# Performance work log

Measured on AMD Instinct MI355X. Metric: run time of the kernel, lower is better.

Reference implementation:

```python
import jax, jax.numpy as jnp
import numpy as np

NUM_HEADS = 16
HEAD_DIM = 128
NUM_KV_HEADS = 8
NUM_KV_GROUPS = 2
HIDDEN = 2048
SCALE = 0.5  # hardcoded in the original SDPA call


def _fixed_sincos_pos(E, H):
    # matches ReusedProjReconstructor._fixed_sincos_pos (H even here)
    half = H // 2
    freq = jnp.exp(-jnp.log(jnp.float32(10000.0)) * jnp.arange(half, dtype=jnp.float32) / half)
    pos = jnp.arange(E, dtype=jnp.float32)[:, None]
    ang = pos * freq[None, :]
    return jnp.concatenate([jnp.sin(ang), jnp.cos(ang)], axis=1)  # [E, H]


def setup_inputs() -> dict:
    key = jax.random.key(0)
    ks = jax.random.split(key, 8)
    B, M, H = 4, 2048, HIDDEN
    kv_dim = NUM_KV_HEADS * HEAD_DIM
    s = 0.02
    return {
        "mem_act": jax.random.normal(ks[0], (B, M, H), jnp.float32),
        "Wq": jax.random.normal(ks[1], (H, H), jnp.float32) * s,
        "bq": jax.random.normal(ks[2], (H,), jnp.float32) * s,
        "Wk": jax.random.normal(ks[3], (kv_dim, H), jnp.float32) * s,
        "bk": jax.random.normal(ks[4], (kv_dim,), jnp.float32) * s,
        "Wv": jax.random.normal(ks[5], (kv_dim, H), jnp.float32) * s,
        "bv": jax.random.normal(ks[6], (kv_dim,), jnp.float32) * s,
        "Wo": jax.random.normal(ks[7], (H, H), jnp.float32) * s,
        "E": 2048,
    }


def reference(mem_act, Wq, bq, Wk, bk, Wv, bv, Wo, E):
    B, M, H = mem_act.shape
    # positional query hidden, shared across batch (q_ln is Identity)
    q_hidden = _fixed_sincos_pos(E, H).astype(mem_act.dtype)  # [E, H]
    q = (q_hidden @ Wq.T + bq).reshape(E, NUM_HEADS, HEAD_DIM)          # [E, nh, hd]
    k = (mem_act @ Wk.T + bk).reshape(B, M, NUM_KV_HEADS, HEAD_DIM)     # [B, M, nkv, hd]
    v = (mem_act @ Wv.T + bv).reshape(B, M, NUM_KV_HEADS, HEAD_DIM)
    # GQA: repeat kv heads (repeat_interleave over head dim)
    k = jnp.repeat(k, NUM_KV_GROUPS, axis=2)  # [B, M, nh, hd]
    v = jnp.repeat(v, NUM_KV_GROUPS, axis=2)
    # non-causal SDPA with scale=0.5, query broadcast over batch
    scores = jnp.einsum("ehd,bmhd->bhem", q, k) * SCALE  # [B, nh, E, M]
    attn = jax.nn.softmax(scores, axis=-1)
    out = jnp.einsum("bhem,bmhd->behd", attn, v).reshape(B, E, H)
    pred = out @ Wo.T  # o_proj (no bias, Qwen2 style)
    return pred
```

## Files before the change

kernel.cpp:

```cpp
#include <hip/hip_runtime.h>
#include <hip/hip_bf16.h>

typedef __attribute__((ext_vector_type(8))) short short8;
typedef __attribute__((ext_vector_type(4))) float f32x4;
typedef __attribute__((ext_vector_type(16))) float f32x16;
typedef unsigned short ushort_t;

__device__ __forceinline__ unsigned short f2bf(float x) {
    unsigned int u = __builtin_bit_cast(unsigned int, x);
    unsigned int r = (u + 0x7fffu + ((u >> 16) & 1u)) >> 16;
    return (unsigned short)r;
}

__device__ __forceinline__ void gload_lds16(const ushort_t* g, ushort_t* l) {
    __builtin_amdgcn_global_load_lds(
        (const __attribute__((address_space(1))) void*)g,
        (__attribute__((address_space(3))) void*)l, 16, 0, 0);
}

#define MFMA16(A, B, C) __builtin_amdgcn_mfma_f32_16x16x32_bf16((A), (B), (C), 0, 0, 0)
#define MFMA32(A, B, C) __builtin_amdgcn_mfma_f32_32x32x16_bf16((A), (B), (C), 0, 0, 0)

__global__ __launch_bounds__(256) void prep_all(const float* __restrict__ im,
                                                const float* __restrict__ iq,
                                                const float* __restrict__ ik,
                                                const float* __restrict__ iv,
                                                const float* __restrict__ io,
                                                ushort_t* __restrict__ om,
                                                ushort_t* __restrict__ oq,
                                                ushort_t* __restrict__ ok,
                                                ushort_t* __restrict__ ov,
                                                ushort_t* __restrict__ oo,
                                                ushort_t* __restrict__ qh) {
    const int bid = blockIdx.x;
    if (bid < 14336) {
        long i = ((long)bid * 256 + threadIdx.x) << 3;
        const float* s;
        ushort_t* d;
        if (i < 16777216)      { s = im + i;              d = om + i; }
        else if (i < 20971520) { s = iq + (i - 16777216); d = oq + (i - 16777216); }
        else if (i < 23068672) { s = ik + (i - 20971520); d = ok + (i - 20971520); }
        else if (i < 25165824) { s = iv + (i - 23068672); d = ov + (i - 23068672); }
        else                   { s = io + (i - 25165824); d = oo + (i - 25165824); }
        const float4* p = (const float4*)s;
        float4 a = p[0], b = p[1];
        short8 o;
        o[0] = (short)f2bf(a.x); o[1] = (short)f2bf(a.y);
        o[2] = (short)f2bf(a.z); o[3] = (short)f2bf(a.w);
        o[4] = (short)f2bf(b.x); o[5] = (short)f2bf(b.y);
        o[6] = (short)f2bf(b.z); o[7] = (short)f2bf(b.w);
        *(short8*)d = o;
    } else {
        int idx = (bid - 14336) * 256 + threadIdx.x;
        int e = idx >> 10, i = idx & 1023;
        float freq = __expf(-9.2103403719761836f * (float)i * (1.0f / 1024.0f));
        float ang = (float)e * freq;
        qh[(size_t)e * 2048 + i]        = f2bf(sinf(ang));
        qh[(size_t)e * 2048 + 1024 + i] = f2bf(cosf(ang));
    }
}

__global__ __launch_bounds__(256) void gemm_q(const ushort_t* __restrict__ A,
                                              const ushort_t* __restrict__ Bw,
                                              const float* __restrict__ bias,
                                              ushort_t* __restrict__ Cout,
                                              int M, int N, int K) {
    __shared__ ushort_t As[128 * 32];
    __shared__ ushort_t Bs[128 * 32];
    const int tid = threadIdx.x;
    const int lane = tid & 63;
    const int wid = tid >> 6;
    const int g = lane >> 4;
    const int r = lane & 15;
    const int wr = wid >> 1, wc = wid & 1;
    const int nbn = N >> 7;
    const int bm = blockIdx.x / nbn, bn = blockIdx.x % nbn;
    const int row0 = bm << 7, col0 = bn << 7;

    f32x4 acc[4][4];
#pragma unroll
    for (int i = 0; i < 4; ++i)
#pragma unroll
        for (int j = 0; j < 4; ++j) acc[i][j] = (f32x4){0.f, 0.f, 0.f, 0.f};

    const int f0 = tid * 8;
    const int r0_ = f0 >> 5, c0_ = f0 & 31;
    const int f1 = (256 + tid) * 8;
    const int r1_ = f1 >> 5, c1_ = f1 & 31;

    for (int k0 = 0; k0 < K; k0 += 32) {
        __syncthreads();
        gload_lds16(A  + (size_t)(row0 + r0_) * K + k0 + c0_, As + f0);
        gload_lds16(A  + (size_t)(row0 + r1_) * K + k0 + c1_, As + f1);
        gload_lds16(Bw + (size_t)(col0 + r0_) * K + k0 + c0_, Bs + f0);
        gload_lds16(Bw + (size_t)(col0 + r1_) * K + k0 + c1_, Bs + f1);
        __syncthreads();
        short8 af[4], bfr[4];
#pragma unroll
        for (int i = 0; i < 4; ++i) {
            af[i]  = *(const short8*)(As + (wr * 64 + i * 16 + r) * 32 + g * 8);
            bfr[i] = *(const short8*)(Bs + (wc * 64 + i * 16 + r) * 32 + g * 8);
        }
#pragma unroll
        for (int i = 0; i < 4; ++i)
#pragma unroll
            for (int j = 0; j < 4; ++j) acc[i][j] = MFMA16(af[i], bfr[j], acc[i][j]);
    }

#pragma unroll
    for (int j = 0; j < 4; ++j) {
        const int col = col0 + wc * 64 + j * 16 + r;
        const float bv = bias[col];
#pragma unroll
        for (int i = 0; i < 4; ++i) {
            const int rowb = row0 + wr * 64 + i * 16 + g * 4;
#pragma unroll
            for (int t = 0; t < 4; ++t) {
                float v = (acc[i][j][t] + bv) * 0.5f;
                Cout[(size_t)(rowb + t) * N + col] = f2bf(v);
            }
        }
    }
}

template <int EPI>
__global__ __launch_bounds__(512, 1) void gemm256(const ushort_t* __restrict__ A,
                                                  const ushort_t* __restrict__ Bw,
                                                  const float* __restrict__ b0,
                                                  const float* __restrict__ b1,
                                                  void* __restrict__ C0,
                                                  void* __restrict__ C1,
                                                  int M, int N, int K) {
    __shared__ ushort_t As[4][256 * 32];
    __shared__ ushort_t Bs[4][256 * 32];
    const int tid = threadIdx.x, lane = tid & 63;
    const int wid = tid >> 6;
    const int q5 = lane & 31, hi = lane >> 5;
    const int wm = wid >> 2, wn = wid & 3;
    const int nbn = N >> 8;
    const int nwg = gridDim.x;
    const int swz = (blockIdx.x & 7) * (nwg >> 3) + (blockIdx.x >> 3);
    const int bm = swz / nbn, bn = swz % nbn;
    const int row0 = bm << 8, col0 = bn << 8;
    const int NT = K >> 5;

    f32x16 acc[4][2];
#pragma unroll
    for (int mi = 0; mi < 4; ++mi)
#pragma unroll
        for (int nj = 0; nj < 2; ++nj)
#pragma unroll
            for (int rr = 0; rr < 16; ++rr) acc[mi][nj][rr] = 0.f;

    auto STAGE_HALF = [&](int buf, int kt, int i) {
        const int k0 = kt << 5;
        const int fb = (i * 512 + tid) << 4;
        const int rp = fb >> 7;
        const int bo = ((fb >> 4) & 7) ^ (rp & 7);
        const int row = rp * 2 + (bo >> 2);
        const int kc = (bo & 3) << 3;
        gload_lds16(A  + (size_t)(row0 + row) * K + k0 + kc, &As[buf][0] + (fb >> 1));
        gload_lds16(Bw + (size_t)(col0 + row) * K + k0 + kc, &Bs[buf][0] + (fb >> 1));
    };

    STAGE_HALF(0, 0, 0); STAGE_HALF(0, 0, 1);
    STAGE_HALF(1, 1, 0); STAGE_HALF(1, 1, 1);
    STAGE_HALF(2, 2, 0); STAGE_HALF(2, 2, 1);
    asm volatile("s_waitcnt vmcnt(8)" ::: "memory");
    __builtin_amdgcn_sched_barrier(0);
    __builtin_amdgcn_s_barrier();
    __builtin_amdgcn_sched_barrier(0);

    for (int t = 0; t < NT; ++t) {
        const int buf = t & 3;
        const char* Ab = (const char*)&As[buf][0];
        const char* Bb = (const char*)&Bs[buf][0];
#pragma unroll
        for (int ph = 0; ph < 2; ++ph) {
            short8 af[4], bfr[2];
#pragma unroll
            for (int nj = 0; nj < 2; ++nj) {
                const int col = wn * 64 + nj * 32 + q5;
                const int rp = col >> 1;
                const int blk = (((col & 1) << 2) + ph * 2 + hi) ^ (rp & 7);
                bfr[nj] = *(const short8*)(Bb + rp * 128 + blk * 16);
            }
#pragma unroll
            for (int mi = 0; mi < 4; ++mi) {
                const int row = wm * 128 + mi * 32 + q5;
                const int rp = row >> 1;
                const int blk = (((row & 1) << 2) + ph * 2 + hi) ^ (rp & 7);
                af[mi] = *(const short8*)(Ab + rp * 128 + blk * 16);
            }
            if (t + 3 < NT) STAGE_HALF((t + 3) & 3, t + 3, ph);
            __builtin_amdgcn_s_setprio(1);
#pragma unroll
            for (int mi = 0; mi < 4; ++mi)
#pragma unroll
                for (int nj = 0; nj < 2; ++nj)
                    acc[mi][nj] = MFMA32(af[mi], bfr[nj], acc[mi][nj]);
            __builtin_amdgcn_s_setprio(0);
        }

        if (t + 3 < NT) {
            asm volatile("s_waitcnt vmcnt(8)" ::: "memory");
        } else if (t + 2 < NT) {
            asm volatile("s_waitcnt vmcnt(4)" ::: "memory");
        } else if (t + 1 < NT) {
            asm volatile("s_waitcnt vmcnt(0)" ::: "memory");
        }
        if (t + 1 < NT) {
            __builtin_amdgcn_sched_barrier(0);
            __builtin_amdgcn_s_barrier();
            __builtin_amdgcn_sched_barrier(0);
        }
    }

#pragma unroll
    for (int mi = 0; mi < 4; ++mi)
#pragma unroll
        for (int nj = 0; nj < 2; ++nj) {
            const int col = col0 + wn * 64 + nj * 32 + q5;
            if (EPI == 2) {
                float* outp = (float*)C0;
#pragma unroll
                for (int rr = 0; rr < 16; ++rr) {
                    const int row = row0 + wm * 128 + mi * 32 + (rr & 3) + 8 * (rr >> 2) + 4 * hi;
                    outp[(size_t)row * N + col] = acc[mi][nj][rr];
                }
            } else {
                if (col < 1024) {
                    const float bv = b0[col];
                    ushort_t* Kp = (ushort_t*)C0;
#pragma unroll
                    for (int rr = 0; rr < 16; ++rr) {
                        const int row = row0 + wm * 128 + mi * 32 + (rr & 3) + 8 * (rr >> 2) + 4 * hi;
                        Kp[(size_t)row * 1024 + col] = f2bf(acc[mi][nj][rr] + bv);
                    }
                } else {
                    const int vcol = col - 1024;
                    const float bv = b1[vcol];
                    ushort_t* Vt = (ushort_t*)C1;
#pragma unroll
                    for (int G = 0; G < 4; ++G) {
                        const int m0 = row0 + wm * 128 + mi * 32 + G * 8 + 4 * hi;
                        const int bb = m0 >> 11;
                        const int mm = m0 & 2047;
                        const size_t vtrow = (size_t)(bb * 8 + (vcol >> 7)) * 128 + (vcol & 127);
                        unsigned int p0 = (unsigned int)f2bf(acc[mi][nj][G * 4 + 0] + bv)
                                        | ((unsigned int)f2bf(acc[mi][nj][G * 4 + 1] + bv) << 16);
                        unsigned int p1 = (unsigned int)f2bf(acc[mi][nj][G * 4 + 2] + bv)
                                        | ((unsigned int)f2bf(acc[mi][nj][G * 4 + 3] + bv) << 16);
                        uint2 pk; pk.x = p0; pk.y = p1;
                        *(uint2*)(Vt + vtrow * 2048 + mm) = pk;
                    }
                }
            }
        }
}

__global__ __launch_bounds__(512, 2) void attn_kernel(const ushort_t* __restrict__ Q,
                                                      const ushort_t* __restrict__ Kg,
                                                      const ushort_t* __restrict__ Vt,
                                                      ushort_t* __restrict__ O) {
    __shared__ ushort_t Ks[2][64 * 128];
    __shared__ ushort_t Vts[2][128 * 64];

    const int tid = threadIdx.x, lane = tid & 63, wid = tid >> 6;
    const int q5 = lane & 31;
    const int hi = lane >> 5;
    const int wq = wid & 3;
    const int wg = (blockIdx.x & 7) * 64 + (blockIdx.x >> 3);
    const int bkvh = wg >> 4;
    const int etile = wg & 15;
    const int b = bkvh >> 3, kvh = bkvh & 7;
    const int h = kvh * 2 + (wid >> 2);
    const int e0 = etile * 128;
    const int qrow = e0 + wq * 32 + q5;

    short8 Qf[8];
    {
        const ushort_t* qp = Q + (size_t)qrow * 2048 + h * 128 + hi * 8;
#pragma unroll
        for (int c = 0; c < 8; ++c) Qf[c] = *(const short8*)(qp + c * 16);
    }

    unsigned aK[2][8];
#pragma unroll
    for (int h2 = 0; h2 < 2; ++h2) {
        const int key = h2 * 32 + q5;
#pragma unroll
        for (int c = 0; c < 8; ++c)
            aK[h2][c] = key * 256 + (((c * 2 + hi) ^ (key & 7)) << 4);
    }
    unsigned aV[4];
#pragma unroll
    for (int c16 = 0; c16 < 4; ++c16)
        aV[c16] = q5 * 128 + (((c16 * 2 + hi) ^ (q5 & 7)) << 4);

    float lrow = 0.f;
    f32x16 oacc[4];
#pragma unroll
    for (int d0 = 0; d0 < 4; ++d0)
#pragma unroll
        for (int r = 0; r < 16; ++r) oacc[d0][r] = 0.f;

    f32x16 Z16;
#pragma unroll
    for (int r = 0; r < 16; ++r) Z16[r] = 0.f;

    const ushort_t* Kbase  = Kg + (size_t)b * 2048 * 1024 + kvh * 128;
    const ushort_t* Vtbase = Vt + (size_t)bkvh * 128 * 2048;

    auto STAGE = [&](int buf, int kv0) {
#pragma unroll
        for (int i = 0; i < 2; ++i) {
            const int fb = (i * 8 + wid) * 1024 + lane * 16;
            const int key = fb >> 8;
            const int blk = (fb >> 4) & 15;
            gload_lds16(Kbase + (size_t)(kv0 + key) * 1024 + ((blk ^ (key & 7)) << 3),
                        &Ks[buf][0] + (fb >> 1));
            const int d = fb >> 7;
            const int kb = (fb >> 4) & 7;
            gload_lds16(Vtbase + (size_t)d * 2048 + kv0 + ((kb ^ (d & 7)) << 3),
                        &Vts[buf][0] + (fb >> 1));
        }
    };

    auto TILE = [&](int bo) {
        f32x16 sS[2];
        __builtin_amdgcn_s_setprio(1);
#pragma unroll
        for (int c = 0; c < 8; ++c) {
            short8 ka0 = *(const short8*)((const char*)Ks + bo + aK[0][c]);
            short8 ka1 = *(const short8*)((const char*)Ks + bo + aK[1][c]);
            sS[0] = MFMA32(ka0, Qf[c], (c == 0) ? Z16 : sS[0]);
            sS[1] = MFMA32(ka1, Qf[c], (c == 0) ? Z16 : sS[1]);
        }
        __builtin_amdgcn_s_setprio(0);

#pragma unroll
        for (int h2 = 0; h2 < 2; ++h2)
#pragma unroll
            for (int r = 0; r < 16; ++r) sS[h2][r] = __expf(sS[h2][r]);

        float ts[16];
#pragma unroll
        for (int i = 0; i < 8; ++i) ts[i] = sS[0][2 * i] + sS[0][2 * i + 1];
#pragma unroll
        for (int i = 0; i < 8; ++i) ts[8 + i] = sS[1][2 * i] + sS[1][2 * i + 1];
#pragma unroll
        for (int s = 8; s > 0; s >>= 1)
#pragma unroll
            for (int i = 0; i < s; ++i) ts[i] += ts[i + s];
        lrow += ts[0] + __shfl_xor(ts[0], 32);

        unsigned int W[2][4][2];
#pragma unroll
        for (int h2 = 0; h2 < 2; ++h2)
#pragma unroll
            for (int q4 = 0; q4 < 4; ++q4)
#pragma unroll
                for (int p = 0; p < 2; ++p) {
                    unsigned int w;
                    asm("v_cvt_pk_bf16_f32 %0, %1, %2"
                        : "=v"(w)
                        : "v"(sS[h2][q4 * 4 + 2 * p]), "v"(sS[h2][q4 * 4 + 2 * p + 1]));
                    W[h2][q4][p] = w;
                }

#pragma unroll
        for (int c16 = 0; c16 < 4; ++c16) {
            const int h2 = c16 >> 1;
            const int q4a = (c16 & 1) * 2, q4b = q4a + 1;
            auto r0 = __builtin_amdgcn_permlane32_swap(W[h2][q4a][0], W[h2][q4b][0], false, false);
            auto r1 = __builtin_amdgcn_permlane32_swap(W[h2][q4a][1], W[h2][q4b][1], false, false);
            union { unsigned int w[4]; short8 v; } pa;
            pa.w[0] = r0[0];
            pa.w[1] = r1[0];
            pa.w[2] = r0[1];
            pa.w[3] = r1[1];
            __builtin_amdgcn_s_setprio(1);
#pragma unroll
            for (int d0 = 0; d0 < 4; ++d0) {
                short8 vb = *(const short8*)((const char*)Vts + bo + aV[c16] + d0 * 4096);
                oacc[d0] = MFMA32(pa.v, vb, oacc[d0]);
            }
            __builtin_amdgcn_s_setprio(0);
        }
    };

    STAGE(0, 0);
    __syncthreads();

#pragma unroll 1
    for (int tt = 0; tt < 16; ++tt) {
        STAGE(1, (2 * tt + 1) * 64);
        TILE(0);
        __syncthreads();
        if (tt < 15) STAGE(0, (2 * tt + 2) * 64);
        TILE(16384);
        __syncthreads();
    }

#pragma unroll
    for (int reg = 0; reg < 16; ++reg) {
        const int qr = (reg & 3) + 8 * (reg >> 2) + 4 * hi;
        const float lr = __shfl(lrow, qr);
        const float inv = 1.0f / lr;
        const int e = e0 + wq * 32 + qr;
        ushort_t* op = O + ((size_t)b * 2048 + e) * 2048 + h * 128 + q5;
#pragma unroll
        for (int d0 = 0; d0 < 4; ++d0)
            op[d0 * 32] = f2bf(oacc[d0][reg] * inv);
    }
}

extern "C" void kernel_launch(void* const* d_in, const int* in_sizes, int n_in,
                              void* d_out, int out_size, void* d_ws, size_t ws_size,
                              hipStream_t stream) {
    const float* mem_act = (const float*)d_in[0];
    const float* Wq = (const float*)d_in[1];
    const float* bq = (const float*)d_in[2];
    const float* Wk = (const float*)d_in[3];
    const float* bk = (const float*)d_in[4];
    const float* Wv = (const float*)d_in[5];
    const float* bv = (const float*)d_in[6];
    const float* Wo = (const float*)d_in[7];
    float* out = (float*)d_out;

    char* w = (char*)d_ws;
    ushort_t* memb = (ushort_t*)w; w += (size_t)16777216 * 2;
    ushort_t* wqb  = (ushort_t*)w; w += (size_t)4194304 * 2;
    ushort_t* wkvb = (ushort_t*)w; w += (size_t)4194304 * 2;
    ushort_t* wob  = (ushort_t*)w; w += (size_t)4194304 * 2;
    ushort_t* qh   = (ushort_t*)w; w += (size_t)4194304 * 2;
    ushort_t* Qp   = (ushort_t*)w; w += (size_t)4194304 * 2;
    ushort_t* Kp   = (ushort_t*)w; w += (size_t)8388608 * 2;
    ushort_t* Vtp  = (ushort_t*)w; w += (size_t)8388608 * 2;
    ushort_t* AO   = (ushort_t*)w; w += (size_t)16777216 * 2;

    dim3 blk(256);
    prep_all<<<22528, blk, 0, stream>>>(mem_act, Wq, Wk, Wv, Wo,
                                        memb, wqb, wkvb, wkvb + (size_t)2097152, wob, qh);

    gemm_q<<<16 * 16, blk, 0, stream>>>(qh, wqb, bq, Qp, 2048, 2048, 2048);

    gemm256<0><<<256, dim3(512), 0, stream>>>(memb, wkvb, bk, bv, Kp, Vtp, 8192, 2048, 2048);

    attn_kernel<<<512, dim3(512), 0, stream>>>(Qp, Kp, Vtp, AO);

    gemm256<2><<<256, dim3(512), 0, stream>>>(AO, wob, nullptr, nullptr, out, nullptr, 8192, 2048, 2048);
}
```

Baseline: 367.8 us.

## Pipeline Q-projection GEMM with 4-stage LDS buffers and 32x32 MFMA

Rewrites the Q projection GEMM to use a 4-buffer LDS ring with loads issued three k-steps ahead, swizzled LDS layout, 32x32x16 MFMA tiles, workgroup index swizzling and setprio around MFMA bursts. This replaces the original single-buffer loop that synchronized twice per k-step. It also swaps sinf/cosf for hardware v_sin/v_cos on range-reduced revolutions when building positional query inputs, which may lose a little precision for large angles. The Q GEMM is small (2048x2048x2048) relative to the whole pipeline, so overall impact is bounded.

```diff
diff --git a/kernel.cpp b/kernel.cpp
--- a/kernel.cpp
+++ b/kernel.cpp
@@ -55,72 +55,118 @@
         int e = idx >> 10, i = idx & 1023;
         float freq = __expf(-9.2103403719761836f * (float)i * (1.0f / 1024.0f));
         float ang = (float)e * freq;
-        qh[(size_t)e * 2048 + i]        = f2bf(sinf(ang));
-        qh[(size_t)e * 2048 + 1024 + i] = f2bf(cosf(ang));
-    }
-}
-
-__global__ __launch_bounds__(256) void gemm_q(const ushort_t* __restrict__ A,
-                                              const ushort_t* __restrict__ Bw,
-                                              const float* __restrict__ bias,
-                                              ushort_t* __restrict__ Cout,
-                                              int M, int N, int K) {
-    __shared__ ushort_t As[128 * 32];
-    __shared__ ushort_t Bs[128 * 32];
-    const int tid = threadIdx.x;
-    const int lane = tid & 63;
+        float rev = ang * 0.15915494309189535f;
+        rev -= floorf(rev);
+        float sv, cv;
+        asm("v_sin_f32 %0, %1" : "=v"(sv) : "v"(rev));
+        asm("v_cos_f32 %0, %1" : "=v"(cv) : "v"(rev));
+        qh[(size_t)e * 2048 + i]        = f2bf(sv);
+        qh[(size_t)e * 2048 + 1024 + i] = f2bf(cv);
+    }
+}
+
+__global__ __launch_bounds__(256, 2) void gemm_q(const ushort_t* __restrict__ A,
+                                                 const ushort_t* __restrict__ Bw,
+                                                 const float* __restrict__ bias,
+                                                 ushort_t* __restrict__ Cout,
+                                                 int M, int N, int K) {
+    __shared__ ushort_t As[4][128 * 32];
+    __shared__ ushort_t Bs[4][128 * 32];
+    const int tid = threadIdx.x, lane = tid & 63;
     const int wid = tid >> 6;
-    const int g = lane >> 4;
-    const int r = lane & 15;
-    const int wr = wid >> 1, wc = wid & 1;
+    const int q5 = lane & 31, hi = lane >> 5;
+    const int wm = wid >> 1, wn = wid & 1;
     const int nbn = N >> 7;
-    const int bm = blockIdx.x / nbn, bn = blockIdx.x % nbn;
+    const int nwg = gridDim.x;
+    const int swz = (blockIdx.x & 7) * (nwg >> 3) + (blockIdx.x >> 3);
+    const int bm = swz / nbn, bn = swz % nbn;
     const int row0 = bm << 7, col0 = bn << 7;
-
-    f32x4 acc[4][4];
-#pragma unroll
-    for (int i = 0; i < 4; ++i)
-#pragma unroll
-        for (int j = 0; j < 4; ++j) acc[i][j] = (f32x4){0.f, 0.f, 0.f, 0.f};
-
-    const int f0 = tid * 8;
-    const int r0_ = f0 >> 5, c0_ = f0 & 31;
-    const int f1 = (256 + tid) * 8;
-    const int r1_ = f1 >> 5, c1_ = f1 & 31;
-
-    for (int k0 = 0; k0 < K; k0 += 32) {
-        __syncthreads();
-        gload_lds16(A  + (size_t)(row0 + r0_) * K + k0 + c0_, As + f0);
-        gload_lds16(A  + (size_t)(row0 + r1_) * K + k0 + c1_, As + f1);
-        gload_lds16(Bw + (size_t)(col0 + r0_) * K + k0 + c0_, Bs + f0);
-        gload_lds16(Bw + (size_t)(col0 + r1_) * K + k0 + c1_, Bs + f1);
-        __syncthreads();
-        short8 af[4], bfr[4];
-#pragma unroll
-        for (int i = 0; i < 4; ++i) {
-            af[i]  = *(const short8*)(As + (wr * 64 + i * 16 + r) * 32 + g * 8);
-            bfr[i] = *(const short8*)(Bs + (wc * 64 + i * 16 + r) * 32 + g * 8);
-        }
-#pragma unroll
-        for (int i = 0; i < 4; ++i)
-#pragma unroll
-            for (int j = 0; j < 4; ++j) acc[i][j] = MFMA16(af[i], bfr[j], acc[i][j]);
-    }
-
-#pragma unroll
-    for (int j = 0; j < 4; ++j) {
-        const int col = col0 + wc * 64 + j * 16 + r;
-        const float bv = bias[col];
-#pragma unroll
-        for (int i = 0; i < 4; ++i) {
-            const int rowb = row0 + wr * 64 + i * 16 + g * 4;
-#pragma unroll
-            for (int t = 0; t < 4; ++t) {
-                float v = (acc[i][j][t] + bv) * 0.5f;
-                Cout[(size_t)(rowb + t) * N + col] = f2bf(v);
-            }
-        }
-    }
+    const int NT = K >> 5;
+
+    f32x16 acc[2][2];
+#pragma unroll
+    for (int mi = 0; mi < 2; ++mi)
+#pragma unroll
+        for (int nj = 0; nj < 2; ++nj)
+#pragma unroll
+            for (int rr = 0; rr < 16; ++rr) acc[mi][nj][rr] = 0.f;
+
+    auto STAGE_HALF = [&](int buf, int kt, int i) {
+        const int k0 = kt << 5;
+        const int fb = (i * 256 + tid) << 4;
+        const int rp = fb >> 7;
+        const int bo = ((fb >> 4) & 7) ^ (rp & 7);
+        const int row = rp * 2 + (bo >> 2);
+        const int kc = (bo & 3) << 3;
+        gload_lds16(A  + (size_t)(row0 + row) * K + k0 + kc, &As[buf][0] + (fb >> 1));
+        gload_lds16(Bw + (size_t)(col0 + row) * K + k0 + kc, &Bs[buf][0] + (fb >> 1));
+    };
+
+    STAGE_HALF(0, 0, 0); STAGE_HALF(0, 0, 1);
+    STAGE_HALF(1, 1, 0); STAGE_HALF(1, 1, 1);
+    STAGE_HALF(2, 2, 0); STAGE_HALF(2, 2, 1);
+    asm volatile("s_waitcnt vmcnt(8)" ::: "memory");
+    __builtin_amdgcn_sched_barrier(0);
+    __builtin_amdgcn_s_barrier();
+    __builtin_amdgcn_sched_barrier(0);
+
+    for (int t = 0; t < NT; ++t) {
+        const int buf = t & 3;
+        const char* Ab = (const char*)&As[buf][0];
+        const char* Bb = (const char*)&Bs[buf][0];
+#pragma unroll
+        for (int ph = 0; ph < 2; ++ph) {
+            short8 af[2], bfr[2];
+#pragma unroll
+            for (int nj = 0; nj < 2; ++nj) {
+                const int col = wn * 64 + nj * 32 + q5;
+                const int rp = col >> 1;
+                const int blk = (((col & 1) << 2) + ph * 2 + hi) ^ (rp & 7);
+                bfr[nj] = *(const short8*)(Bb + rp * 128 + blk * 16);
+            }
+#pragma unroll
+            for (int mi = 0; mi < 2; ++mi) {
+                const int row = wm * 64 + mi * 32 + q5;
+                const int rp = row >> 1;
+                const int blk = (((row & 1) << 2) + ph * 2 + hi) ^ (rp & 7);
+                af[mi] = *(const short8*)(Ab + rp * 128 + blk * 16);
+            }
+            if (t + 3 < NT) STAGE_HALF((t + 3) & 3, t + 3, ph);
+            __builtin_amdgcn_s_setprio(1);
+#pragma unroll
+            for (int mi = 0; mi < 2; ++mi)
+#pragma unroll
+                for (int nj = 0; nj < 2; ++nj)
+                    acc[mi][nj] = MFMA32(af[mi], bfr[nj], acc[mi][nj]);
+            __builtin_amdgcn_s_setprio(0);
+        }
+
+        if (t + 3 < NT) {
+            asm volatile("s_waitcnt vmcnt(8)" ::: "memory");
+        } else if (t + 2 < NT) {
+            asm volatile("s_waitcnt vmcnt(4)" ::: "memory");
+        } else if (t + 1 < NT) {
+            asm volatile("s_waitcnt vmcnt(0)" ::: "memory");
+        }
+        if (t + 1 < NT) {
+            __builtin_amdgcn_sched_barrier(0);
+            __builtin_amdgcn_s_barrier();
+            __builtin_amdgcn_sched_barrier(0);
+        }
+    }
+
+#pragma unroll
+    for (int mi = 0; mi < 2; ++mi)
+#pragma unroll
+        for (int nj = 0; nj < 2; ++nj) {
+            const int col = col0 + wn * 64 + nj * 32 + q5;
+            const float bv = bias[col];
+#pragma unroll
+            for (int rr = 0; rr < 16; ++rr) {
+                const int row = row0 + wm * 64 + mi * 32 + (rr & 3) + 8 * (rr >> 2) + 4 * hi;
+                Cout[(size_t)row * N + col] = f2bf((acc[mi][nj][rr] + bv) * 0.5f);
+            }
+        }
 }
 
 template <int EPI>
```

Result: no change. 363.3 us (-1.2%).
